# Kernel optimization log

Hardware: AMD Instinct MI355X
Metric: run time of the kernel (lower is better)

The kernel has to match this reference:

```python
import jax, jax.numpy as jnp
import numpy as np

L, H, D, BINS = 4, 8, 512, 16
HD = D // H
DFF = 4 * D
EPS = 1e-5


def _ln(x, g, b):
    mu = jnp.mean(x, axis=-1, keepdims=True)
    var = jnp.var(x, axis=-1, keepdims=True)
    return (x - mu) * jax.lax.rsqrt(var + EPS) * g + b


def setup_inputs() -> dict:
    key = jax.random.key(0)
    ks = jax.random.split(key, 24)
    B, N, F = 8, 1024, 4
    s = 0.02
    inp = {
        'slot_features': jax.random.normal(ks[0], (B, N, F), jnp.float32),
        'distance_matrix': jax.random.uniform(ks[1], (B, N, N), jnp.float32),
        'slot_mask': jnp.ones((B, N), dtype=bool),
        # input projection (Linear 4->D, then ReLU, then LayerNorm)
        'in_w': jax.random.normal(ks[2], (F, D), jnp.float32) * s,
        'in_b': jnp.zeros((D,), jnp.float32),
        'in_g': jnp.ones((D,), jnp.float32),
        'in_beta': jnp.zeros((D,), jnp.float32),
        # learnable distance bias, init linspace(0,-2) per head
        'dist_bias': jnp.tile(jnp.linspace(0.0, -2.0, BINS, dtype=jnp.float32)[None, :], (H, 1)),
        # per-layer stacked params (weights stored [in,out])
        'qkv_w': jax.random.normal(ks[3], (L, D, 3 * D), jnp.float32) * s,
        'qkv_b': jnp.zeros((L, 3 * D), jnp.float32),
        'out_w': jax.random.normal(ks[4], (L, D, D), jnp.float32) * s,
        'out_b': jnp.zeros((L, D), jnp.float32),
        'ffn_w1': jax.random.normal(ks[5], (L, D, DFF), jnp.float32) * s,
        'ffn_b1': jnp.zeros((L, DFF), jnp.float32),
        'ffn_w2': jax.random.normal(ks[6], (L, DFF, D), jnp.float32) * s,
        'ffn_b2': jnp.zeros((L, D), jnp.float32),
        'n1_g': jnp.ones((L, D), jnp.float32),
        'n1_b': jnp.zeros((L, D), jnp.float32),
        'n2_g': jnp.ones((L, D), jnp.float32),
        'n2_b': jnp.zeros((L, D), jnp.float32),
        'op_w': jax.random.normal(ks[7], (D, D), jnp.float32) * s,
        'op_b': jnp.zeros((D,), jnp.float32),
    }
    return inp


def _distance_bias(distance_matrix, slot_mask, dist_bias):
    # (B,H,N,N) additive attention bias from binned normalized distances
    max_dist = jnp.clip(jnp.max(distance_matrix, axis=(-1, -2), keepdims=True), 1e-6, None)
    norm_dist = distance_matrix / max_dist
    bin_idx = jnp.clip((norm_dist * (BINS - 1)).astype(jnp.int32), 0, BINS - 1)  # (B,N,N)
    bias = jnp.transpose(dist_bias.T[bin_idx], (0, 3, 1, 2))  # (B,N,N,H)->(B,H,N,N)
    pad = ~(slot_mask[:, :, None] & slot_mask[:, None, :])  # (B,N,N)
    return jnp.where(pad[:, None, :, :], -jnp.inf, bias)


def reference(slot_features, distance_matrix, slot_mask, in_w, in_b, in_g, in_beta,
              dist_bias, qkv_w, qkv_b, out_w, out_b, ffn_w1, ffn_b1, ffn_w2, ffn_b2,
              n1_g, n1_b, n2_g, n2_b, op_w, op_b):
    B, N, _ = slot_features.shape
    h = _ln(jax.nn.relu(slot_features @ in_w + in_b), in_g, in_beta)  # (B,N,D)
    attn_bias = _distance_bias(distance_matrix, slot_mask, dist_bias)  # (B,H,N,N)
    scale = 1.0 / jnp.sqrt(jnp.float32(HD))
    for i in range(L):
        hn = _ln(h, n1_g[i], n1_b[i])
        qkv = (hn @ qkv_w[i] + qkv_b[i]).reshape(B, N, 3, H, HD)
        q, k, v = (jnp.transpose(qkv[:, :, j], (0, 2, 1, 3)) for j in range(3))  # (B,H,N,HD)
        scores = jnp.einsum('bhnd,bhmd->bhnm', q, k) * scale + attn_bias
        attn = jax.nn.softmax(scores, axis=-1)
        o = jnp.einsum('bhnm,bhmd->bhnd', attn, v)
        o = jnp.transpose(o, (0, 2, 1, 3)).reshape(B, N, D)
        h = h + (o @ out_w[i] + out_b[i])
        hn2 = _ln(h, n2_g[i], n2_b[i])
        ff = jax.nn.gelu(hn2 @ ffn_w1[i] + ffn_b1[i], approximate=False) @ ffn_w2[i] + ffn_b2[i]
        h = h + ff
    return h @ op_w + op_b
```

## Files before the change

kernel.cpp:

```cpp
#include <hip/hip_runtime.h>


typedef __attribute__((ext_vector_type(8))) short short8;
typedef __attribute__((ext_vector_type(4))) float f32x4;

__device__ __forceinline__ float b2f(unsigned short u){
  return __uint_as_float(((unsigned)u) << 16);
}
__device__ __forceinline__ unsigned short f2b(float f){
  unsigned u = __float_as_uint(f);
  u += 0x7fffU + ((u >> 16) & 1U);
  return (unsigned short)(u >> 16);
}
__device__ __forceinline__ void gload16(const void* g, void* l){
  __builtin_amdgcn_global_load_lds((const __attribute__((address_space(1))) void*)g,
                                   (__attribute__((address_space(3))) void*)l, 16, 0, 0);
}

__global__ void transpose_w(const float* __restrict__ src, unsigned short* __restrict__ dst,
                            int K, int N){
  __shared__ float tile[32][33];
  const float* s = src + (size_t)blockIdx.z * K * N;
  unsigned short* d = dst + (size_t)blockIdx.z * K * N;
  int j = threadIdx.x & 31, i0 = threadIdx.x >> 5;
  int kt = blockIdx.y * 32, nt = blockIdx.x * 32;
#pragma unroll
  for (int s4 = 0; s4 < 4; ++s4){
    int i = i0 + s4 * 8;
    tile[i][j] = s[(size_t)(kt + i) * N + nt + j];
  }
  __syncthreads();
#pragma unroll
  for (int s4 = 0; s4 < 4; ++s4){
    int i = i0 + s4 * 8;
    d[(size_t)(nt + i) * K + kt + j] = f2b(tile[j][i]);
  }
}

__global__ void bmax_kernel(const float* __restrict__ dist, unsigned* __restrict__ bmax){
  int b = blockIdx.x >> 5, sl = blockIdx.x & 31;
  const float* p = dist + (size_t)b * 1048576 + sl * 32768;
  int t = threadIdx.x;
  float m = 0.f;
  for (int i = t * 4; i < 32768; i += 1024){
    float4 v = *(const float4*)(p + i);
    m = fmaxf(m, fmaxf(fmaxf(v.x, v.y), fmaxf(v.z, v.w)));
  }
#pragma unroll
  for (int o = 1; o < 64; o <<= 1) m = fmaxf(m, __shfl_xor(m, o));
  __shared__ float wm[4];
  if ((t & 63) == 0) wm[t >> 6] = m;
  __syncthreads();
  if (t == 0){
    m = fmaxf(fmaxf(wm[0], wm[1]), fmaxf(wm[2], wm[3]));
    atomicMax(bmax + b, __float_as_uint(m));
  }
}

__global__ void bins_kernel(const float* __restrict__ dist, const unsigned* __restrict__ bmax,
                            unsigned char* __restrict__ out){
  int idx = (blockIdx.x * 256 + threadIdx.x) * 4;
  int b = idx >> 20;
  float mx = fmaxf(__uint_as_float(bmax[b]), 1e-6f);
  float4 v = *(const float4*)(dist + idx);
  int b0 = (int)((v.x / mx) * 15.0f); b0 = b0 < 0 ? 0 : (b0 > 15 ? 15 : b0);
  int b1 = (int)((v.y / mx) * 15.0f); b1 = b1 < 0 ? 0 : (b1 > 15 ? 15 : b1);
  int b2 = (int)((v.z / mx) * 15.0f); b2 = b2 < 0 ? 0 : (b2 > 15 ? 15 : b2);
  int b3 = (int)((v.w / mx) * 15.0f); b3 = b3 < 0 ? 0 : (b3 > 15 ? 15 : b3);
  uchar4 o; o.x = (unsigned char)b0; o.y = (unsigned char)b1; o.z = (unsigned char)b2; o.w = (unsigned char)b3;
  *(uchar4*)(out + idx) = o;
}

__global__ void inproj_kernel(const float* __restrict__ x, const float* __restrict__ w,
                              const float* __restrict__ b, const float* __restrict__ g,
                              const float* __restrict__ be, float* __restrict__ h){
  int t = threadIdx.x, wv = t >> 6, lane = t & 63;
  int row = blockIdx.x * 4 + wv;
  float x0 = x[row * 4 + 0], x1 = x[row * 4 + 1], x2 = x[row * 4 + 2], x3 = x[row * 4 + 3];
  int c0 = lane * 4, c1 = 256 + lane * 4;
  float4 v0, v1; float s = 0.f, sq = 0.f;
  {
    float4 w0 = *(const float4*)(w + c0), w1 = *(const float4*)(w + 512 + c0);
    float4 w2 = *(const float4*)(w + 1024 + c0), w3 = *(const float4*)(w + 1536 + c0);
    float4 bb = *(const float4*)(b + c0);
    v0.x = fmaxf(0.f, x0*w0.x + x1*w1.x + x2*w2.x + x3*w3.x + bb.x);
    v0.y = fmaxf(0.f, x0*w0.y + x1*w1.y + x2*w2.y + x3*w3.y + bb.y);
    v0.z = fmaxf(0.f, x0*w0.z + x1*w1.z + x2*w2.z + x3*w3.z + bb.z);
    v0.w = fmaxf(0.f, x0*w0.w + x1*w1.w + x2*w2.w + x3*w3.w + bb.w);
    s += v0.x + v0.y + v0.z + v0.w;
    sq += v0.x*v0.x + v0.y*v0.y + v0.z*v0.z + v0.w*v0.w;
  }
  {
    float4 w0 = *(const float4*)(w + c1), w1 = *(const float4*)(w + 512 + c1);
    float4 w2 = *(const float4*)(w + 1024 + c1), w3 = *(const float4*)(w + 1536 + c1);
    float4 bb = *(const float4*)(b + c1);
    v1.x = fmaxf(0.f, x0*w0.x + x1*w1.x + x2*w2.x + x3*w3.x + bb.x);
    v1.y = fmaxf(0.f, x0*w0.y + x1*w1.y + x2*w2.y + x3*w3.y + bb.y);
    v1.z = fmaxf(0.f, x0*w0.z + x1*w1.z + x2*w2.z + x3*w3.z + bb.z);
    v1.w = fmaxf(0.f, x0*w0.w + x1*w1.w + x2*w2.w + x3*w3.w + bb.w);
    s += v1.x + v1.y + v1.z + v1.w;
    sq += v1.x*v1.x + v1.y*v1.y + v1.z*v1.z + v1.w*v1.w;
  }
#pragma unroll
  for (int o = 1; o < 64; o <<= 1){ s += __shfl_xor(s, o); sq += __shfl_xor(sq, o); }
  float mu = s * (1.f / 512.f);
  float var = sq * (1.f / 512.f) - mu * mu;
  float rs = rsqrtf(var + 1e-5f);
  float* hp = h + (size_t)row * 512;
  {
    float4 gg = *(const float4*)(g + c0), bb = *(const float4*)(be + c0);
    float4 o4;
    o4.x = (v0.x - mu) * rs * gg.x + bb.x; o4.y = (v0.y - mu) * rs * gg.y + bb.y;
    o4.z = (v0.z - mu) * rs * gg.z + bb.z; o4.w = (v0.w - mu) * rs * gg.w + bb.w;
    *(float4*)(hp + c0) = o4;
  }
  {
    float4 gg = *(const float4*)(g + c1), bb = *(const float4*)(be + c1);
    float4 o4;
    o4.x = (v1.x - mu) * rs * gg.x + bb.x; o4.y = (v1.y - mu) * rs * gg.y + bb.y;
    o4.z = (v1.z - mu) * rs * gg.z + bb.z; o4.w = (v1.w - mu) * rs * gg.w + bb.w;
    *(float4*)(hp + c1) = o4;
  }
}

__global__ void ln_kernel(const float* __restrict__ h, const float* __restrict__ g,
                          const float* __restrict__ b, unsigned short* __restrict__ out){
  int t = threadIdx.x, wv = t >> 6, lane = t & 63;
  int row = blockIdx.x * 4 + wv;
  const float* hp = h + (size_t)row * 512;
  int c0 = lane * 4, c1 = 256 + lane * 4;
  float4 u0 = *(const float4*)(hp + c0);
  float4 u1 = *(const float4*)(hp + c1);
  float s = u0.x + u0.y + u0.z + u0.w + u1.x + u1.y + u1.z + u1.w;
  float sq = u0.x*u0.x + u0.y*u0.y + u0.z*u0.z + u0.w*u0.w
           + u1.x*u1.x + u1.y*u1.y + u1.z*u1.z + u1.w*u1.w;
#pragma unroll
  for (int o = 1; o < 64; o <<= 1){ s += __shfl_xor(s, o); sq += __shfl_xor(sq, o); }
  float mu = s * (1.f / 512.f);
  float var = sq * (1.f / 512.f) - mu * mu;
  float rs = rsqrtf(var + 1e-5f);
  unsigned short* op = out + (size_t)row * 512;
  {
    float4 gg = *(const float4*)(g + c0), bb = *(const float4*)(b + c0);
    ushort4 o4;
    o4.x = f2b((u0.x - mu) * rs * gg.x + bb.x); o4.y = f2b((u0.y - mu) * rs * gg.y + bb.y);
    o4.z = f2b((u0.z - mu) * rs * gg.z + bb.z); o4.w = f2b((u0.w - mu) * rs * gg.w + bb.w);
    *(ushort4*)(op + c0) = o4;
  }
  {
    float4 gg = *(const float4*)(g + c1), bb = *(const float4*)(b + c1);
    ushort4 o4;
    o4.x = f2b((u1.x - mu) * rs * gg.x + bb.x); o4.y = f2b((u1.y - mu) * rs * gg.y + bb.y);
    o4.z = f2b((u1.z - mu) * rs * gg.z + bb.z); o4.w = f2b((u1.w - mu) * rs * gg.w + bb.w);
    *(ushort4*)(op + c1) = o4;
  }
}

#define EPI_BF 0
#define EPI_RESID 1
#define EPI_GELU 2
#define EPI_RESID_BF 3
#define EPI_F32 4

template<int N, int K, int EPI>
__global__ __launch_bounds__(256) void gemm_k(
    const unsigned short* __restrict__ A,
    const unsigned short* __restrict__ Bt,
    const float* __restrict__ bias,
    float* __restrict__ resid,
    unsigned short* __restrict__ outb,
    float* __restrict__ outf)
{
  __shared__ unsigned short As[4096], Bs[4096];
  int t = threadIdx.x, w = t >> 6, lane = t & 63;
  int l15 = lane & 15, g = lane >> 4;
  int bm = blockIdx.x, bn = blockIdx.y;
  int wm = w >> 1, wn = w & 1;
  f32x4 acc[4][4];
#pragma unroll
  for (int i = 0; i < 4; ++i)
#pragma unroll
    for (int j = 0; j < 4; ++j) acc[i][j] = (f32x4){0.f, 0.f, 0.f, 0.f};

  for (int kt = 0; kt < K / 32; ++kt){
#pragma unroll
    for (int it = 0; it < 2; ++it){
      int ci = it * 4 + w;
      int o = ci * 1024 + lane * 16;
      int row = o >> 6, sp = (o >> 4) & 3;
      int sl = sp ^ ((row >> 1) & 3);
      gload16(A + (size_t)(bm * 128 + row) * K + kt * 32 + sl * 8, As + ci * 512);
      gload16(Bt + (size_t)(bn * 128 + row) * K + kt * 32 + sl * 8, Bs + ci * 512);
    }
    __syncthreads();
    short8 af[4], bf[4];
#pragma unroll
    for (int i = 0; i < 4; ++i){
      int row = wm * 64 + i * 16 + l15;
      int sp = g ^ ((row >> 1) & 3);
      af[i] = *(const short8*)(As + row * 32 + sp * 8);
    }
#pragma unroll
    for (int j = 0; j < 4; ++j){
      int row = wn * 64 + j * 16 + l15;
      int sp = g ^ ((row >> 1) & 3);
      bf[j] = *(const short8*)(Bs + row * 32 + sp * 8);
    }
#pragma unroll
    for (int i = 0; i < 4; ++i)
#pragma unroll
      for (int j = 0; j < 4; ++j)
        acc[i][j] = __builtin_amdgcn_mfma_f32_16x16x32_bf16(af[i], bf[j], acc[i][j], 0, 0, 0);
    __syncthreads();
  }
  int rbase = bm * 128 + wm * 64, cbase = bn * 128 + wn * 64;
#pragma unroll
  for (int j = 0; j < 4; ++j){
    int col = cbase + j * 16 + l15;
    float bs = bias[col];
#pragma unroll
    for (int i = 0; i < 4; ++i){
#pragma unroll
      for (int r = 0; r < 4; ++r){
        int row = rbase + i * 16 + g * 4 + r;
        size_t idx = (size_t)row * N + col;
        float x = acc[i][j][r] + bs;
        if constexpr (EPI == EPI_BF){
          outb[idx] = f2b(x);
        } else if constexpr (EPI == EPI_RESID){
          resid[idx] = resid[idx] + x;
        } else if constexpr (EPI == EPI_GELU){
          float y = 0.5f * x * (1.f + erff(x * 0.70710678118654752f));
          outb[idx] = f2b(y);
        } else if constexpr (EPI == EPI_RESID_BF){
          float y = resid[idx] + x;
          resid[idx] = y;
          outb[idx] = f2b(y);
        } else {
          outf[idx] = x;
        }
      }
    }
  }
}

__global__ __launch_bounds__(256) void attn_kernel(
    const unsigned short* __restrict__ qkv,
    const unsigned char* __restrict__ bins,
    const float* __restrict__ dist_bias,
    unsigned short* __restrict__ o_out)
{
  __shared__ unsigned short Ks[64 * 72];
  __shared__ unsigned short Vt[64 * 72];
  __shared__ unsigned short Ps[4][16 * 72];
  int qt = blockIdx.x, bh = blockIdx.y;
  int b = bh >> 3, h = bh & 7;
  int t = threadIdx.x, w = t >> 6, lane = t & 63;
  int l15 = lane & 15, g = lane >> 4;
  unsigned short* Psw = Ps[w];
  float lutv = dist_bias[h * 16 + l15];

  int qrow_frag = qt * 64 + w * 16 + l15;
  const unsigned short* qp = qkv + ((size_t)(b * 1024 + qrow_frag)) * 1536 + h * 64;
  short8 qf[2];
#pragma unroll
  for (int c = 0; c < 2; ++c){
    short8 raw = *(const short8*)(qp + c * 32 + g * 8);
#pragma unroll
    for (int e = 0; e < 8; ++e)
      raw[e] = (short)f2b(b2f((unsigned short)raw[e]) * 0.125f);
    qf[c] = raw;
  }

  float m_run[4], l_run[4];
  f32x4 acc_o[4];
#pragma unroll
  for (int r = 0; r < 4; ++r){ m_run[r] = -1e30f; l_run[r] = 0.f; }
#pragma unroll
  for (int d = 0; d < 4; ++d) acc_o[d] = (f32x4){0.f, 0.f, 0.f, 0.f};

  int qrow_c = qt * 64 + w * 16 + g * 4;
  int srow = t >> 3, sslot = t & 7;

  for (int kt = 0; kt < 16; ++kt){
    __syncthreads();
#pragma unroll
    for (int half = 0; half < 2; ++half){
      int sr = srow + half * 32;
      const unsigned short* kp = qkv + ((size_t)(b * 1024 + kt * 64 + sr)) * 1536 + 512 + h * 64 + sslot * 8;
      *(short8*)(Ks + sr * 72 + sslot * 8) = *(const short8*)kp;
      short8 vv = *(const short8*)(kp + 512);
#pragma unroll
      for (int e = 0; e < 8; ++e)
        Vt[(sslot * 8 + e) * 72 + sr] = (unsigned short)vv[e];
    }
    __syncthreads();

    f32x4 sv[4];
#pragma unroll
    for (int ks = 0; ks < 4; ++ks){
      f32x4 a = (f32x4){0.f, 0.f, 0.f, 0.f};
#pragma unroll
      for (int c = 0; c < 2; ++c){
        short8 kf = *(const short8*)(Ks + (ks * 16 + l15) * 72 + c * 32 + g * 8);
        a = __builtin_amdgcn_mfma_f32_16x16x32_bf16(qf[c], kf, a, 0, 0, 0);
      }
      sv[ks] = a;
    }
#pragma unroll
    for (int r = 0; r < 4; ++r){
      const unsigned char* bp = bins + ((size_t)(b * 1024 + qrow_c + r)) * 1024 + kt * 64 + l15;
#pragma unroll
      for (int ks = 0; ks < 4; ++ks){
        int bin = bp[ks * 16];
        sv[ks][r] += __shfl(lutv, bin);
      }
    }
    float mt[4];
#pragma unroll
    for (int r = 0; r < 4; ++r)
      mt[r] = fmaxf(fmaxf(sv[0][r], sv[1][r]), fmaxf(sv[2][r], sv[3][r]));
#pragma unroll
    for (int o = 1; o < 16; o <<= 1)
#pragma unroll
      for (int r = 0; r < 4; ++r) mt[r] = fmaxf(mt[r], __shfl_xor(mt[r], o));
    float mnew[4], alpha[4];
#pragma unroll
    for (int r = 0; r < 4; ++r){
      mnew[r] = fmaxf(m_run[r], mt[r]);
      alpha[r] = __expf(m_run[r] - mnew[r]);
      m_run[r] = mnew[r];
    }
    float rs_[4] = {0.f, 0.f, 0.f, 0.f};
#pragma unroll
    for (int ks = 0; ks < 4; ++ks)
#pragma unroll
      for (int r = 0; r < 4; ++r){
        float p = __expf(sv[ks][r] - mnew[r]);
        rs_[r] += p;
        Psw[(g * 4 + r) * 72 + ks * 16 + l15] = f2b(p);
      }
#pragma unroll
    for (int o = 1; o < 16; o <<= 1)
#pragma unroll
      for (int r = 0; r < 4; ++r) rs_[r] += __shfl_xor(rs_[r], o);
#pragma unroll
    for (int r = 0; r < 4; ++r) l_run[r] = l_run[r] * alpha[r] + rs_[r];
#pragma unroll
    for (int d = 0; d < 4; ++d){
      f32x4 ao = acc_o[d];
#pragma unroll
      for (int r = 0; r < 4; ++r) ao[r] *= alpha[r];
      acc_o[d] = ao;
    }
#pragma unroll
    for (int c = 0; c < 2; ++c){
      short8 pa = *(const short8*)(Psw + l15 * 72 + c * 32 + g * 8);
#pragma unroll
      for (int d = 0; d < 4; ++d){
        short8 vf = *(const short8*)(Vt + (d * 16 + l15) * 72 + c * 32 + g * 8);
        acc_o[d] = __builtin_amdgcn_mfma_f32_16x16x32_bf16(pa, vf, acc_o[d], 0, 0, 0);
      }
    }
  }
#pragma unroll
  for (int d = 0; d < 4; ++d)
#pragma unroll
    for (int r = 0; r < 4; ++r){
      float v = acc_o[d][r] / l_run[r];
      size_t row = (size_t)(b * 1024 + qrow_c + r);
      o_out[row * 512 + h * 64 + d * 16 + l15] = f2b(v);
    }
}

extern "C" void kernel_launch(void* const* d_in, const int* in_sizes, int n_in,
                              void* d_out, int out_size, void* d_ws, size_t ws_size,
                              hipStream_t stream) {
  const float* x     = (const float*)d_in[0];
  const float* dist  = (const float*)d_in[1];
  const float* in_w  = (const float*)d_in[3];
  const float* in_b  = (const float*)d_in[4];
  const float* in_g  = (const float*)d_in[5];
  const float* in_be = (const float*)d_in[6];
  const float* dbias = (const float*)d_in[7];
  const float* qkv_w = (const float*)d_in[8];
  const float* qkv_b = (const float*)d_in[9];
  const float* out_w = (const float*)d_in[10];
  const float* out_b = (const float*)d_in[11];
  const float* f1_w  = (const float*)d_in[12];
  const float* f1_b  = (const float*)d_in[13];
  const float* f2_w  = (const float*)d_in[14];
  const float* f2_b  = (const float*)d_in[15];
  const float* n1g   = (const float*)d_in[16];
  const float* n1b   = (const float*)d_in[17];
  const float* n2g   = (const float*)d_in[18];
  const float* n2b   = (const float*)d_in[19];
  const float* op_w  = (const float*)d_in[20];
  const float* op_b  = (const float*)d_in[21];

  char* ws = (char*)d_ws;
  size_t off = 0;
  auto alloc = [&](size_t bytes){ size_t o = off; off += (bytes + 255) & ~(size_t)255; return o; };
  unsigned short* wqkv  = (unsigned short*)(ws + alloc((size_t)4 * 1536 * 512 * 2));
  unsigned short* wout  = (unsigned short*)(ws + alloc((size_t)4 * 512 * 512 * 2));
  unsigned short* wf1   = (unsigned short*)(ws + alloc((size_t)4 * 2048 * 512 * 2));
  unsigned short* wf2   = (unsigned short*)(ws + alloc((size_t)4 * 512 * 2048 * 2));
  unsigned short* wop   = (unsigned short*)(ws + alloc((size_t)512 * 512 * 2));
  float*          h     = (float*)(ws + alloc((size_t)8192 * 512 * 4));
  unsigned short* actbf = (unsigned short*)(ws + alloc((size_t)8192 * 512 * 2));
  unsigned short* qkvff = (unsigned short*)(ws + alloc((size_t)8192 * 2048 * 2));
  unsigned char*  binsb = (unsigned char*)(ws + alloc((size_t)8 * 1024 * 1024));
  unsigned*       bmax  = (unsigned*)(ws + alloc(256));
  (void)ws_size; (void)in_sizes; (void)n_in; (void)out_size;

  hipMemsetAsync(bmax, 0, 32, stream);
  transpose_w<<<dim3(48, 16, 4), 256, 0, stream>>>(qkv_w, wqkv, 512, 1536);
  transpose_w<<<dim3(16, 16, 4), 256, 0, stream>>>(out_w, wout, 512, 512);
  transpose_w<<<dim3(64, 16, 4), 256, 0, stream>>>(f1_w, wf1, 512, 2048);
  transpose_w<<<dim3(16, 64, 4), 256, 0, stream>>>(f2_w, wf2, 2048, 512);
  transpose_w<<<dim3(16, 16, 1), 256, 0, stream>>>(op_w, wop, 512, 512);
  bmax_kernel<<<256, 256, 0, stream>>>(dist, bmax);
  bins_kernel<<<8192, 256, 0, stream>>>(dist, bmax, binsb);
  inproj_kernel<<<2048, 256, 0, stream>>>(x, in_w, in_b, in_g, in_be, h);

  for (int l = 0; l < 4; ++l){
    ln_kernel<<<2048, 256, 0, stream>>>(h, n1g + l * 512, n1b + l * 512, actbf);
    gemm_k<1536, 512, EPI_BF><<<dim3(64, 12), 256, 0, stream>>>(
        actbf, wqkv + (size_t)l * 1536 * 512, qkv_b + l * 1536, nullptr, qkvff, nullptr);
    attn_kernel<<<dim3(16, 64), 256, 0, stream>>>(qkvff, binsb, dbias, actbf);
    gemm_k<512, 512, EPI_RESID><<<dim3(64, 4), 256, 0, stream>>>(
        actbf, wout + (size_t)l * 512 * 512, out_b + l * 512, h, nullptr, nullptr);
    ln_kernel<<<2048, 256, 0, stream>>>(h, n2g + l * 512, n2b + l * 512, actbf);
    gemm_k<2048, 512, EPI_GELU><<<dim3(64, 16), 256, 0, stream>>>(
        actbf, wf1 + (size_t)l * 2048 * 512, f1_b + l * 2048, nullptr, qkvff, nullptr);
    gemm_k<512, 2048, EPI_RESID_BF><<<dim3(64, 4), 256, 0, stream>>>(
        qkvff, wf2 + (size_t)l * 512 * 2048, f2_b + l * 512, h, actbf, nullptr);
  }
  gemm_k<512, 512, EPI_F32><<<dim3(64, 4), 256, 0, stream>>>(
      actbf, wop, op_b, nullptr, nullptr, (float*)d_out);
}
```

Measured before the change: 1.113 ms.

## Pretranspose V and stream K/V tiles into swizzled LDS via direct loads

Adds a separate kernel that writes V transposed per (batch, head) into spare workspace, so the attention kernel can load K and V tiles with global_load_lds directly into LDS. The padded LDS layouts are replaced by XOR-swizzled 64-wide layouts to avoid bank conflicts, and distance bins are read as 32-bit words and spread across lanes with shuffles instead of byte loads. The grid order is also swapped so consecutive blocks cover different batch/head pairs. This removes the scalar scatter transpose of V inside attention, at the cost of an extra launch and an extra pass over V in global memory.

```diff
diff --git a/kernel.cpp b/kernel.cpp
--- a/kernel.cpp
+++ b/kernel.cpp
@@ -34,6 +34,24 @@
   for (int s4 = 0; s4 < 4; ++s4){
     int i = i0 + s4 * 8;
     d[(size_t)(nt + i) * K + kt + j] = f2b(tile[j][i]);
+  }
+}
+
+__global__ void vt_kernel(const unsigned short* __restrict__ qkv, unsigned short* __restrict__ vt){
+  __shared__ unsigned short tile[32][33];
+  int tt = blockIdx.x, dt = blockIdx.y, bh = blockIdx.z;
+  int b = bh >> 3, h = bh & 7;
+  int j = threadIdx.x & 31, i0 = threadIdx.x >> 5;
+#pragma unroll
+  for (int s4 = 0; s4 < 4; ++s4){
+    int i = i0 + s4 * 8;
+    tile[i][j] = qkv[(size_t)(b * 1024 + tt * 32 + i) * 1536 + 1024 + h * 64 + dt * 32 + j];
+  }
+  __syncthreads();
+#pragma unroll
+  for (int s4 = 0; s4 < 4; ++s4){
+    int i = i0 + s4 * 8;
+    vt[(size_t)(bh * 64 + dt * 32 + i) * 1024 + tt * 32 + j] = tile[j][i];
   }
 }
 
@@ -246,17 +264,19 @@
 
 __global__ __launch_bounds__(256) void attn_kernel(
     const unsigned short* __restrict__ qkv,
+    const unsigned short* __restrict__ vt,
     const unsigned char* __restrict__ bins,
     const float* __restrict__ dist_bias,
     unsigned short* __restrict__ o_out)
 {
-  __shared__ unsigned short Ks[64 * 72];
-  __shared__ unsigned short Vt[64 * 72];
-  __shared__ unsigned short Ps[4][16 * 72];
-  int qt = blockIdx.x, bh = blockIdx.y;
-  int b = bh >> 3, h = bh & 7;
+  __shared__ unsigned short Ks[64 * 64];
+  __shared__ unsigned short Vs[64 * 64];
+  __shared__ unsigned short Ps[4][16 * 64];
+  int bhx = blockIdx.x, qt = blockIdx.y;
+  int b = bhx & 7, h = bhx >> 3;
+  int bh = b * 8 + h;
   int t = threadIdx.x, w = t >> 6, lane = t & 63;
-  int l15 = lane & 15, g = lane >> 4;
+  int l15 = lane & 15, g = lane >> 4, rx = lane & 7;
   unsigned short* Psw = Ps[w];
   float lutv = dist_bias[h * 16 + l15];
 
@@ -280,19 +300,20 @@
   for (int d = 0; d < 4; ++d) acc_o[d] = (f32x4){0.f, 0.f, 0.f, 0.f};
 
   int qrow_c = qt * 64 + w * 16 + g * 4;
-  int srow = t >> 3, sslot = t & 7;
+  int srow_lo = lane >> 3;
+  int sslot = lane & 7;
 
   for (int kt = 0; kt < 16; ++kt){
     __syncthreads();
 #pragma unroll
-    for (int half = 0; half < 2; ++half){
-      int sr = srow + half * 32;
-      const unsigned short* kp = qkv + ((size_t)(b * 1024 + kt * 64 + sr)) * 1536 + 512 + h * 64 + sslot * 8;
-      *(short8*)(Ks + sr * 72 + sslot * 8) = *(const short8*)kp;
-      short8 vv = *(const short8*)(kp + 512);
-#pragma unroll
-      for (int e = 0; e < 8; ++e)
-        Vt[(sslot * 8 + e) * 72 + sr] = (unsigned short)vv[e];
+    for (int it = 0; it < 2; ++it){
+      int ci = it * 4 + w;
+      int row = ci * 8 + srow_lo;
+      int sl = sslot ^ (row & 7);
+      gload16(qkv + (size_t)(b * 1024 + kt * 64 + row) * 1536 + 512 + h * 64 + sl * 8,
+              Ks + ci * 512);
+      gload16(vt + (size_t)(bh * 64 + row) * 1024 + kt * 64 + sl * 8,
+              Vs + ci * 512);
     }
     __syncthreads();
 
@@ -302,20 +323,23 @@
       f32x4 a = (f32x4){0.f, 0.f, 0.f, 0.f};
 #pragma unroll
       for (int c = 0; c < 2; ++c){
-        short8 kf = *(const short8*)(Ks + (ks * 16 + l15) * 72 + c * 32 + g * 8);
+        short8 kf = *(const short8*)(Ks + (ks * 16 + l15) * 64 + ((c * 4 + g) ^ rx) * 8);
         a = __builtin_amdgcn_mfma_f32_16x16x32_bf16(qf[c], kf, a, 0, 0, 0);
       }
       sv[ks] = a;
     }
-#pragma unroll
-    for (int r = 0; r < 4; ++r){
-      const unsigned char* bp = bins + ((size_t)(b * 1024 + qrow_c + r)) * 1024 + kt * 64 + l15;
+    unsigned bw[4];
+#pragma unroll
+    for (int r = 0; r < 4; ++r)
+      bw[r] = *(const unsigned*)(bins + (size_t)(b * 1024 + qrow_c + r) * 1024 + kt * 64 + l15 * 4);
+#pragma unroll
+    for (int r = 0; r < 4; ++r)
 #pragma unroll
       for (int ks = 0; ks < 4; ++ks){
-        int bin = bp[ks * 16];
+        unsigned word = __shfl(bw[r], g * 16 + ks * 4 + (l15 >> 2));
+        int bin = (word >> ((l15 & 3) * 8)) & 255;
         sv[ks][r] += __shfl(lutv, bin);
       }
-    }
     float mt[4];
 #pragma unroll
     for (int r = 0; r < 4; ++r)
@@ -338,7 +362,8 @@
       for (int r = 0; r < 4; ++r){
         float p = __expf(sv[ks][r] - mnew[r]);
         rs_[r] += p;
-        Psw[(g * 4 + r) * 72 + ks * 16 + l15] = f2b(p);
+        int prow = g * 4 + r;
+        Psw[prow * 64 + ((ks * 2 + (l15 >> 3)) ^ (prow & 7)) * 8 + (l15 & 7)] = f2b(p);
       }
 #pragma unroll
     for (int o = 1; o < 16; o <<= 1)
@@ -355,10 +380,10 @@
     }
 #pragma unroll
     for (int c = 0; c < 2; ++c){
-      short8 pa = *(const short8*)(Psw + l15 * 72 + c * 32 + g * 8);
+      short8 pa = *(const short8*)(Psw + l15 * 64 + ((c * 4 + g) ^ rx) * 8);
 #pragma unroll
       for (int d = 0; d < 4; ++d){
-        short8 vf = *(const short8*)(Vt + (d * 16 + l15) * 72 + c * 32 + g * 8);
+        short8 vf = *(const short8*)(Vs + (d * 16 + l15) * 64 + ((c * 4 + g) ^ rx) * 8);
         acc_o[d] = __builtin_amdgcn_mfma_f32_16x16x32_bf16(pa, vf, acc_o[d], 0, 0, 0);
       }
     }
@@ -411,6 +436,7 @@
   unsigned short* qkvff = (unsigned short*)(ws + alloc((size_t)8192 * 2048 * 2));
   unsigned char*  binsb = (unsigned char*)(ws + alloc((size_t)8 * 1024 * 1024));
   unsigned*       bmax  = (unsigned*)(ws + alloc(256));
+  unsigned short* vt    = qkvff + (size_t)8192 * 1536;
   (void)ws_size; (void)in_sizes; (void)n_in; (void)out_size;
 
   hipMemsetAsync(bmax, 0, 32, stream);
@@ -427,7 +453,8 @@
     ln_kernel<<<2048, 256, 0, stream>>>(h, n1g + l * 512, n1b + l * 512, actbf);
     gemm_k<1536, 512, EPI_BF><<<dim3(64, 12), 256, 0, stream>>>(
         actbf, wqkv + (size_t)l * 1536 * 512, qkv_b + l * 1536, nullptr, qkvff, nullptr);
-    attn_kernel<<<dim3(16, 64), 256, 0, stream>>>(qkvff, binsb, dbias, actbf);
+    vt_kernel<<<dim3(32, 2, 64), 256, 0, stream>>>(qkvff, vt);
+    attn_kernel<<<dim3(64, 16), 256, 0, stream>>>(qkvff, vt, binsb, dbias, actbf);
     gemm_k<512, 512, EPI_RESID><<<dim3(64, 4), 256, 0, stream>>>(
         actbf, wout + (size_t)l * 512 * 512, out_b + l * 512, h, nullptr, nullptr);
     ln_kernel<<<2048, 256, 0, stream>>>(h, n2g + l * 512, n2b + l * 512, actbf);
```

Result: faster. 1.076 ms (-3.4%).
